# Optimization experiments

Hardware: AMD Instinct MI355X
Metric: run time of the kernel (lower is better)

Reference implementation:

```python
import jax, jax.numpy as jnp
import numpy as np

N, C_IN, P, S_D = 8, 512, 64, 512
N_GROUPS = C_IN // P      # 8
C_OUT = C_IN              # c_out defaults to c_in
EPS = 1e-5                # F.instance_norm default
SLOPE = 0.01              # LeakyReLU default


def setup_inputs() -> dict:
    key = jax.random.key(0)
    ks = jax.random.split(key, 8)
    def xavier(k, shape):
        fan_out, fan_in = shape
        std = (2.0 / (fan_in + fan_out)) ** 0.5
        return jax.random.normal(k, shape, dtype=jnp.float32) * std
    return {
        "style_encoding": jax.random.normal(ks[0], (N, S_D, 32, 32), dtype=jnp.float32),
        "predicted": jax.random.normal(ks[1], (N, C_IN, 128, 128), dtype=jnp.float32),
        "W1": xavier(ks[2], (C_IN, S_D)),
        "b1": jnp.full((C_IN,), 0.01, dtype=jnp.float32),
        "W2": xavier(ks[3], (C_OUT * P, C_IN)),
        "b2": jnp.full((C_OUT * P,), 0.01, dtype=jnp.float32),
        "Wb1": xavier(ks[4], (C_IN, S_D)),
        "bb1": jnp.full((C_IN,), 0.01, dtype=jnp.float32),
        "Wb2": xavier(ks[5], (C_OUT, C_IN)),
        "bb2": jnp.full((C_OUT,), 0.01, dtype=jnp.float32),
    }


def _forward(style_encoding, predicted, W1, b1, W2, b2, Wb1, bb1, Wb2, bb2):
    n, c, h, w = predicted.shape
    # AdaptiveAvgPool2d(1): pooled style vector [N, s_d]
    s = jnp.mean(style_encoding, axis=(2, 3))
    # kernel branch: two 1x1 convs on a 1x1 map == two matmuls
    hk = jax.nn.leaky_relu(s @ W1.T + b1, SLOPE)
    kn = hk @ W2.T + b2                      # [N, c_out*p]
    kernel = kn.reshape(n, N_GROUPS, P, P)   # row n*c_out+oc -> (n, oc//p, oc%p, :)
    # bias branch
    hb = jax.nn.leaky_relu(s @ Wb1.T + bb1, SLOPE)
    bias = (hb @ Wb2.T + bb2).reshape(n, N_GROUPS, P)  # [N, n_groups, p]
    # instance norm (no affine, biased variance)
    mu = jnp.mean(predicted, axis=(2, 3), keepdims=True)
    var = jnp.var(predicted, axis=(2, 3), keepdims=True)
    xn = (predicted - mu) * jax.lax.rsqrt(var + EPS)
    # grouped 1x1 conv: per (sample, group) GEMM [p,p] x [p, H*W]
    xg = xn.reshape(n, N_GROUPS, P, h, w)
    out = jnp.einsum("ngop,ngphw->ngohw", kernel, xg) + bias[:, :, :, None, None]
    return out.reshape(n, C_OUT, h, w)


def reference(style_encoding, predicted, W1, b1, W2, b2, Wb1, bb1, Wb2, bb2):
    return _forward(style_encoding, predicted, W1, b1, W2, b2, Wb1, bb1, Wb2, bb2)
```

## Files before the change

### kernel.cpp

```cpp
#include <hip/hip_runtime.h>


typedef __attribute__((ext_vector_type(8))) short bf16x8;
typedef __attribute__((ext_vector_type(4))) float f32x4;

__device__ __forceinline__ float lrelu(float v) { return v > 0.f ? v : 0.01f * v; }

__device__ __forceinline__ unsigned short f2bf(float f) {
    unsigned int u = __float_as_uint(f);
    unsigned int r = (u + 0x7FFFu + ((u >> 16) & 1u)) >> 16;
    return (unsigned short)r;
}

__global__ void k_pool(const float* __restrict__ style, float* __restrict__ s) {
    int wv = threadIdx.x >> 6, lane = threadIdx.x & 63;
    int b = blockIdx.x * 4 + wv;
    const float4* p4 = (const float4*)(style + (size_t)b * 1024);
    float v = 0.f;
    #pragma unroll
    for (int i = 0; i < 4; ++i) {
        float4 t = p4[lane + 64 * i];
        v += t.x + t.y + t.z + t.w;
    }
    #pragma unroll
    for (int off = 32; off > 0; off >>= 1) v += __shfl_xor(v, off, 64);
    if (lane == 0) s[b] = v * (1.f / 1024.f);
}

__global__ void k_mlp1(const float* __restrict__ s, const float* __restrict__ W1,
                       const float* __restrict__ b1, const float* __restrict__ Wb1,
                       const float* __restrict__ bb1, float* __restrict__ hk,
                       float* __restrict__ hb) {
    __shared__ float sv[4096];
    const float4* s4 = (const float4*)s;
    float4* sv4 = (float4*)sv;
    #pragma unroll
    for (int i = 0; i < 4; ++i) sv4[threadIdx.x + 256 * i] = s4[threadIdx.x + 256 * i];
    __syncthreads();
    int wv = threadIdx.x >> 6, lane = threadIdx.x & 63;
    int row = blockIdx.x * 4 + wv;
    int r2 = row & 511;
    const float* wrow = (row < 512) ? W1 + (size_t)r2 * 512 : Wb1 + (size_t)r2 * 512;
    float bias = (row < 512) ? b1[r2] : bb1[r2];
    float acc[8] = {0.f,0.f,0.f,0.f,0.f,0.f,0.f,0.f};
    #pragma unroll
    for (int c = 0; c < 2; ++c) {
        float4 w4 = *(const float4*)(wrow + lane * 4 + 256 * c);
        #pragma unroll
        for (int n = 0; n < 8; ++n) {
            float4 h4 = *(const float4*)(sv + n * 512 + lane * 4 + 256 * c);
            acc[n] += w4.x * h4.x + w4.y * h4.y + w4.z * h4.z + w4.w * h4.w;
        }
    }
    #pragma unroll
    for (int n = 0; n < 8; ++n) {
        float v = acc[n];
        #pragma unroll
        for (int off = 32; off > 0; off >>= 1) v += __shfl_xor(v, off, 64);
        acc[n] = v;
    }
    if (lane == 0) {
        float* dst = (row < 512) ? hk : hb;
        #pragma unroll
        for (int n = 0; n < 8; ++n) dst[n * 512 + r2] = lrelu(acc[n] + bias);
    }
}

__global__ void k_mlp2(const float* __restrict__ hk, const float* __restrict__ hb,
                       const float* __restrict__ W2, const float* __restrict__ b2,
                       const float* __restrict__ Wb2, const float* __restrict__ bb2,
                       float* __restrict__ kn, float* __restrict__ bvec) {
    __shared__ float h[8192];
    const float4* hk4 = (const float4*)hk;
    const float4* hb4 = (const float4*)hb;
    float4* h4 = (float4*)h;
    #pragma unroll
    for (int i = 0; i < 4; ++i) {
        h4[threadIdx.x + 256 * i]        = hk4[threadIdx.x + 256 * i];
        h4[1024 + threadIdx.x + 256 * i] = hb4[threadIdx.x + 256 * i];
    }
    __syncthreads();
    int wv = threadIdx.x >> 6, lane = threadIdx.x & 63;
    int row = blockIdx.x * 4 + wv;
    const float* wrow;
    const float* hbase;
    float bias;
    int r2 = row - 32768;
    if (row < 32768) { wrow = W2 + (size_t)row * 512; hbase = h; bias = b2[row]; }
    else             { wrow = Wb2 + (size_t)r2 * 512; hbase = h + 4096; bias = bb2[r2]; }
    float acc[8] = {0.f,0.f,0.f,0.f,0.f,0.f,0.f,0.f};
    #pragma unroll
    for (int c = 0; c < 2; ++c) {
        float4 w4 = *(const float4*)(wrow + lane * 4 + 256 * c);
        #pragma unroll
        for (int n = 0; n < 8; ++n) {
            float4 x4 = *(const float4*)(hbase + n * 512 + lane * 4 + 256 * c);
            acc[n] += w4.x * x4.x + w4.y * x4.y + w4.z * x4.z + w4.w * x4.w;
        }
    }
    #pragma unroll
    for (int n = 0; n < 8; ++n) {
        float v = acc[n];
        #pragma unroll
        for (int off = 32; off > 0; off >>= 1) v += __shfl_xor(v, off, 64);
        acc[n] = v;
    }
    if (lane == 0) {
        if (row < 32768) {
            #pragma unroll
            for (int n = 0; n < 8; ++n) kn[(size_t)n * 32768 + row] = acc[n] + bias;
        } else {
            #pragma unroll
            for (int n = 0; n < 8; ++n) bvec[n * 512 + r2] = acc[n] + bias;
        }
    }
}

__global__ void k_stats(const float* __restrict__ x, float* __restrict__ mu,
                        float* __restrict__ rs) {
    __shared__ float ps[4], pq[4];
    int b = blockIdx.x;
    int tid = threadIdx.x, wv = tid >> 6, lane = tid & 63;
    const float4* p4 = (const float4*)(x + (size_t)b * 16384);
    float s = 0.f, q = 0.f;
    #pragma unroll
    for (int i = 0; i < 16; ++i) {
        float4 v = p4[tid + 256 * i];
        s += v.x + v.y + v.z + v.w;
        q += v.x * v.x + v.y * v.y + v.z * v.z + v.w * v.w;
    }
    #pragma unroll
    for (int off = 32; off > 0; off >>= 1) {
        s += __shfl_xor(s, off, 64);
        q += __shfl_xor(q, off, 64);
    }
    if (lane == 0) { ps[wv] = s; pq[wv] = q; }
    __syncthreads();
    if (tid == 0) {
        float S = ps[0] + ps[1] + ps[2] + ps[3];
        float Q = pq[0] + pq[1] + pq[2] + pq[3];
        float m = S * (1.f / 16384.f);
        float v = Q * (1.f / 16384.f) - m * m;
        mu[b] = m;
        rs[b] = rsqrtf(v + 1e-5f);
    }
}

__global__ void k_fold(const float* __restrict__ kn, const float* __restrict__ bvec,
                       const float* __restrict__ mu, const float* __restrict__ rs,
                       unsigned short* __restrict__ Kp, float* __restrict__ bp) {
    int wv = threadIdx.x >> 6, lane = threadIdx.x & 63;
    int t = blockIdx.x * 4 + wv;
    int n = t >> 9, rem = t & 511, g = rem >> 6;
    int ci = n * 512 + g * 64 + lane;
    float kv = kn[(size_t)n * 32768 + (size_t)rem * 64 + lane] * rs[ci];
    Kp[(size_t)t * 64 + lane] = f2bf(kv);
    float pm = kv * mu[ci];
    #pragma unroll
    for (int off = 32; off > 0; off >>= 1) pm += __shfl_xor(pm, off, 64);
    if (lane == 0) bp[t] = bvec[n * 512 + rem] - pm;
}

__global__ __launch_bounds__(256) void k_conv(const float* __restrict__ x,
                                              const unsigned short* __restrict__ Kp,
                                              const float* __restrict__ bp,
                                              float* __restrict__ out) {
    int bid = 4095 - (int)blockIdx.x;
    int ng = bid >> 6, slab = bid & 63;
    int wv = threadIdx.x >> 6, lane = threadIdx.x & 63;
    int l15 = lane & 15, lg = lane >> 4;

    const unsigned short* kpb = Kp + (size_t)ng * 4096;
    bf16x8 kfr[4][2];
    #pragma unroll
    for (int ob = 0; ob < 4; ++ob)
        #pragma unroll
        for (int kk = 0; kk < 2; ++kk)
            kfr[ob][kk] = *(const bf16x8*)(kpb + (ob * 16 + l15) * 64 + kk * 32 + lg * 8);

    float bias[4];
    #pragma unroll
    for (int ob = 0; ob < 4; ++ob)
        bias[ob] = bp[ng * 64 + ob * 16 + l15];

    const size_t xbase = (size_t)ng * 64 * 16384;
    int px0 = slab * 256 + wv * 64;

    #pragma unroll
    for (int c = 0; c < 4; ++c) {
        int pxb = px0 + c * 16;
        bf16x8 afr[2];
        #pragma unroll
        for (int kk = 0; kk < 2; ++kk)
            #pragma unroll
            for (int j = 0; j < 8; ++j) {
                int p = kk * 32 + lg * 8 + j;
                afr[kk][j] = (short)f2bf(x[xbase + (size_t)p * 16384 + pxb + l15]);
            }
        #pragma unroll
        for (int ob = 0; ob < 4; ++ob) {
            f32x4 acc = { bias[ob], bias[ob], bias[ob], bias[ob] };
            acc = __builtin_amdgcn_mfma_f32_16x16x32_bf16(afr[0], kfr[ob][0], acc, 0, 0, 0);
            acc = __builtin_amdgcn_mfma_f32_16x16x32_bf16(afr[1], kfr[ob][1], acc, 0, 0, 0);
            f32x4* dst = (f32x4*)(out + (size_t)(ng * 64 + ob * 16 + l15) * 16384 + pxb + lg * 4);
            __builtin_nontemporal_store(acc, dst);
        }
    }
}

extern "C" void kernel_launch(void* const* d_in, const int* in_sizes, int n_in,
                              void* d_out, int out_size, void* d_ws, size_t ws_size,
                              hipStream_t stream) {
    const float* style = (const float*)d_in[0];
    const float* pred  = (const float*)d_in[1];
    const float* W1    = (const float*)d_in[2];
    const float* b1    = (const float*)d_in[3];
    const float* W2    = (const float*)d_in[4];
    const float* b2    = (const float*)d_in[5];
    const float* Wb1   = (const float*)d_in[6];
    const float* bb1   = (const float*)d_in[7];
    const float* Wb2   = (const float*)d_in[8];
    const float* bb2   = (const float*)d_in[9];
    float* out = (float*)d_out;

    float* ws   = (float*)d_ws;
    float* s    = ws;
    float* hk   = s + 4096;
    float* hb   = hk + 4096;
    float* kn   = hb + 4096;
    float* bvec = kn + 262144;
    float* mu   = bvec + 4096;
    float* rs   = mu + 4096;
    float* bp   = rs + 4096;
    unsigned short* Kp = (unsigned short*)(bp + 4096);

    k_pool <<<1024, 256, 0, stream>>>(style, s);
    k_mlp1 <<<256,  256, 0, stream>>>(s, W1, b1, Wb1, bb1, hk, hb);
    k_mlp2 <<<8320, 256, 0, stream>>>(hk, hb, W2, b2, Wb2, bb2, kn, bvec);
    k_stats<<<4096, 256, 0, stream>>>(pred, mu, rs);
    k_fold <<<1024, 256, 0, stream>>>(kn, bvec, mu, rs, Kp, bp);
    k_conv <<<4096, 256, 0, stream>>>(pred, Kp, bp, out);
}
```

Measured before the change: 191.8 us.

## Fuse stats pass with bf16 pixel-major transpose of input for conv

Replaces the per-channel stats kernel with a kernel that reads the input once, computes partial sums per 256-pixel tile, and writes a bf16 copy transposed to pixel-major layout through shared memory. A small reduce kernel then finishes mean and rstd. The conv kernel now loads contiguous bf16x8 fragments instead of doing strided scalar fp32 loads and converting them. This adds a 64 MB intermediate write and read, traded against the uncoalesced access of the second read of the input.

```diff
diff --git a/kernel.cpp b/kernel.cpp
--- a/kernel.cpp
+++ b/kernel.cpp
@@ -116,33 +116,67 @@
     }
 }
 
-__global__ void k_stats(const float* __restrict__ x, float* __restrict__ mu,
-                        float* __restrict__ rs) {
-    __shared__ float ps[4], pq[4];
-    int b = blockIdx.x;
-    int tid = threadIdx.x, wv = tid >> 6, lane = tid & 63;
-    const float4* p4 = (const float4*)(x + (size_t)b * 16384);
-    float s = 0.f, q = 0.f;
-    #pragma unroll
+__global__ __launch_bounds__(256) void k_xpose(const float* __restrict__ x,
+                                               unsigned short* __restrict__ xbf,
+                                               float* __restrict__ part_s,
+                                               float* __restrict__ part_q) {
+    __shared__ unsigned short xs16[256 * 66];
+    int ng = blockIdx.x >> 6, t = blockIdx.x & 63;
+    int tid = threadIdx.x, w = tid >> 6, lane = tid & 63;
+    int px0 = t * 256;
+    #pragma unroll 4
     for (int i = 0; i < 16; ++i) {
-        float4 v = p4[tid + 256 * i];
-        s += v.x + v.y + v.z + v.w;
-        q += v.x * v.x + v.y * v.y + v.z * v.z + v.w * v.w;
-    }
+        int c = i * 4 + w;
+        float4 v = *(const float4*)(x + ((size_t)(ng * 64 + c)) * 16384 + px0 + lane * 4);
+        float s = v.x + v.y + v.z + v.w;
+        float q = v.x * v.x + v.y * v.y + v.z * v.z + v.w * v.w;
+        #pragma unroll
+        for (int off = 32; off > 0; off >>= 1) {
+            s += __shfl_xor(s, off, 64);
+            q += __shfl_xor(q, off, 64);
+        }
+        if (lane == 0) {
+            part_s[(ng * 64 + c) * 64 + t] = s;
+            part_q[(ng * 64 + c) * 64 + t] = q;
+        }
+        int pxl = lane * 4;
+        xs16[(pxl + 0) * 66 + c] = f2bf(v.x);
+        xs16[(pxl + 1) * 66 + c] = f2bf(v.y);
+        xs16[(pxl + 2) * 66 + c] = f2bf(v.z);
+        xs16[(pxl + 3) * 66 + c] = f2bf(v.w);
+    }
+    __syncthreads();
+    unsigned short* ob = xbf + ((size_t)ng * 16384 + px0) * 64;
+    #pragma unroll
+    for (int j = 0; j < 8; ++j) {
+        int idx = j * 256 + tid;
+        int pxl = idx >> 3, pg = (idx & 7) * 8;
+        const unsigned short* src = &xs16[pxl * 66 + pg];
+        uint4 val;
+        val.x = *(const unsigned int*)(src + 0);
+        val.y = *(const unsigned int*)(src + 2);
+        val.z = *(const unsigned int*)(src + 4);
+        val.w = *(const unsigned int*)(src + 6);
+        *(uint4*)(ob + (size_t)pxl * 64 + pg) = val;
+    }
+}
+
+__global__ void k_reduce(const float* __restrict__ part_s, const float* __restrict__ part_q,
+                         float* __restrict__ mu, float* __restrict__ rs) {
+    int w = threadIdx.x >> 6, lane = threadIdx.x & 63;
+    int ch = blockIdx.x * 4 + w;
+    float s = part_s[ch * 64 + lane];
+    float q = part_q[ch * 64 + lane];
     #pragma unroll
     for (int off = 32; off > 0; off >>= 1) {
         s += __shfl_xor(s, off, 64);
         q += __shfl_xor(q, off, 64);
     }
-    if (lane == 0) { ps[wv] = s; pq[wv] = q; }
-    __syncthreads();
-    if (tid == 0) {
-        float S = ps[0] + ps[1] + ps[2] + ps[3];
-        float Q = pq[0] + pq[1] + pq[2] + pq[3];
-        float m = S * (1.f / 16384.f);
-        float v = Q * (1.f / 16384.f) - m * m;
-        mu[b] = m;
-        rs[b] = rsqrtf(v + 1e-5f);
+    if (lane == 0) {
+        float m = s * (1.f / 16384.f);
+        float v = q * (1.f / 16384.f) - m * m;
+        mu[ch] = m;
+        rs[ch] = rsqrtf(v + 1e-5f);
     }
 }
 
@@ -161,7 +195,7 @@
     if (lane == 0) bp[t] = bvec[n * 512 + rem] - pm;
 }
 
-__global__ __launch_bounds__(256) void k_conv(const float* __restrict__ x,
+__global__ __launch_bounds__(256) void k_conv(const unsigned short* __restrict__ xbf,
                                               const unsigned short* __restrict__ Kp,
                                               const float* __restrict__ bp,
                                               float* __restrict__ out) {
@@ -183,20 +217,16 @@
     for (int ob = 0; ob < 4; ++ob)
         bias[ob] = bp[ng * 64 + ob * 16 + l15];
 
-    const size_t xbase = (size_t)ng * 64 * 16384;
+    const unsigned short* xgb = xbf + (size_t)ng * 1048576;
     int px0 = slab * 256 + wv * 64;
 
     #pragma unroll
     for (int c = 0; c < 4; ++c) {
         int pxb = px0 + c * 16;
+        const unsigned short* xp = xgb + (size_t)(pxb + l15) * 64;
         bf16x8 afr[2];
-        #pragma unroll
-        for (int kk = 0; kk < 2; ++kk)
-            #pragma unroll
-            for (int j = 0; j < 8; ++j) {
-                int p = kk * 32 + lg * 8 + j;
-                afr[kk][j] = (short)f2bf(x[xbase + (size_t)p * 16384 + pxb + l15]);
-            }
+        afr[0] = *(const bf16x8*)(xp + lg * 8);
+        afr[1] = *(const bf16x8*)(xp + 32 + lg * 8);
         #pragma unroll
         for (int ob = 0; ob < 4; ++ob) {
             f32x4 acc = { bias[ob], bias[ob], bias[ob], bias[ob] };
@@ -223,21 +253,25 @@
     const float* bb2   = (const float*)d_in[9];
     float* out = (float*)d_out;
 
-    float* ws   = (float*)d_ws;
-    float* s    = ws;
-    float* hk   = s + 4096;
-    float* hb   = hk + 4096;
-    float* kn   = hb + 4096;
-    float* bvec = kn + 262144;
-    float* mu   = bvec + 4096;
-    float* rs   = mu + 4096;
-    float* bp   = rs + 4096;
+    float* ws    = (float*)d_ws;
+    float* s     = ws;
+    float* hk    = s + 4096;
+    float* hb    = hk + 4096;
+    float* kn    = hb + 4096;
+    float* bvec  = kn + 262144;
+    float* mu    = bvec + 4096;
+    float* rs    = mu + 4096;
+    float* bp    = rs + 4096;
     unsigned short* Kp = (unsigned short*)(bp + 4096);
-
-    k_pool <<<1024, 256, 0, stream>>>(style, s);
-    k_mlp1 <<<256,  256, 0, stream>>>(s, W1, b1, Wb1, bb1, hk, hb);
-    k_mlp2 <<<8320, 256, 0, stream>>>(hk, hb, W2, b2, Wb2, bb2, kn, bvec);
-    k_stats<<<4096, 256, 0, stream>>>(pred, mu, rs);
-    k_fold <<<1024, 256, 0, stream>>>(kn, bvec, mu, rs, Kp, bp);
-    k_conv <<<4096, 256, 0, stream>>>(pred, Kp, bp, out);
-}
+    float* part_s = (float*)(Kp + 262144);
+    float* part_q = part_s + 262144;
+    unsigned short* xbf = (unsigned short*)(part_q + 262144);
+
+    k_pool  <<<1024, 256, 0, stream>>>(style, s);
+    k_mlp1  <<<256,  256, 0, stream>>>(s, W1, b1, Wb1, bb1, hk, hb);
+    k_mlp2  <<<8320, 256, 0, stream>>>(hk, hb, W2, b2, Wb2, bb2, kn, bvec);
+    k_xpose <<<4096, 256, 0, stream>>>(pred, xbf, part_s, part_q);
+    k_reduce<<<1024, 256, 0, stream>>>(part_s, part_q, mu, rs);
+    k_fold  <<<1024, 256, 0, stream>>>(kn, bvec, mu, rs, Kp, bp);
+    k_conv  <<<4096, 256, 0, stream>>>(xbf, Kp, bp, out);
+}
```

After: 228.5 us. 19.1% more time.
